# Kernel tuning notes

Hardware: AMD Instinct MI355X
Metric: run time of the kernel (lower is better)

The kernel has to match this reference:

```python
import jax, jax.numpy as jnp
import numpy as np

N_NODES = 50000
N_EDGES = 400000
IN_DIM = 512
OUT_DIM = 128
EPS = 1e-12  # F.normalize eps


def setup_inputs() -> dict:
    key = jax.random.key(0)
    ks = jax.random.split(key, 8)
    x = jax.random.normal(ks[0], (N_NODES, IN_DIM), dtype=jnp.float32)
    edge_index = jax.random.randint(ks[1], (2, N_EDGES), 0, N_NODES, dtype=jnp.int64)
    def glorot(k, fan_in, fan_out):
        s = jnp.sqrt(6.0 / (fan_in + fan_out)).astype(jnp.float32)
        return jax.random.uniform(k, (fan_in, fan_out), jnp.float32, -s, s)
    return {
        "x": x,
        "edge_index": edge_index,
        "W1": glorot(ks[2], IN_DIM, 512), "b1": jnp.zeros((512,), jnp.float32),
        "W2": glorot(ks[3], 512, 256),    "b2": jnp.zeros((256,), jnp.float32),
        "W3": glorot(ks[4], 256, OUT_DIM), "b3": jnp.zeros((OUT_DIM,), jnp.float32),
    }


def _gcn_layer(x, W, b, src, dst, dinv):
    # PyG GCNConv: h = x @ W; propagate with sym-norm D^-1/2 (A+I) D^-1/2; out += bias
    h = x @ W                                   # [N, F_out] dense GEMM (compute core)
    coef = dinv[src] * dinv[dst]                # [E]
    msg = h[src] * coef[:, None]                # gather + scale  [E, F_out]
    agg = jnp.zeros_like(h).at[dst].add(msg)    # scatter-add over destination nodes
    agg = agg + h * (dinv * dinv)[:, None]      # self-loop contribution
    return agg + b


def reference(x, edge_index, W1, b1, W2, b2, W3, b3):
    src, dst = edge_index[0], edge_index[1]
    n = x.shape[0]
    # degree with self-loops: deg[i] = 1 + in-degree(i)
    deg = jnp.ones((n,), x.dtype).at[dst].add(1.0)
    dinv = jax.lax.rsqrt(deg)
    # eval mode: F.dropout(training=False) is identity
    z = jax.nn.relu(_gcn_layer(x, W1, b1, src, dst, dinv))
    z = jax.nn.relu(_gcn_layer(z, W2, b2, src, dst, dinv))
    z = jax.nn.relu(_gcn_layer(z, W3, b3, src, dst, dinv))
    z = z / jnp.sum(z)
    z = jnp.tanh(z) ** 2
    norm = jnp.maximum(jnp.linalg.norm(z, axis=1, keepdims=True), EPS)
    return z / norm
```

## Files before the change

kernel.cpp:

```cpp
#include <hip/hip_runtime.h>
#include <math.h>

#define NN 50000
#define NE 400000
#define SLOTS 48
#define MT 391
#define BXPG 49

typedef unsigned short u16;
typedef __bf16 bf16x8 __attribute__((ext_vector_type(8)));
typedef float f32x4 __attribute__((ext_vector_type(4)));
typedef u16 bfu8 __attribute__((ext_vector_type(8)));
typedef u16 bfu4 __attribute__((ext_vector_type(4)));

__device__ __forceinline__ u16 f2bf(float f) {
    unsigned u = __builtin_bit_cast(unsigned, f);
    u += 0x7fff + ((u >> 16) & 1);
    return (u16)(u >> 16);
}
__device__ __forceinline__ float bf2f(u16 h) {
    unsigned u = ((unsigned)h) << 16;
    return __builtin_bit_cast(float, u);
}
__device__ __forceinline__ bfu8 cvt8(const float4& a, const float4& b) {
    bfu8 o;
    o[0] = f2bf(a.x); o[1] = f2bf(a.y); o[2] = f2bf(a.z); o[3] = f2bf(a.w);
    o[4] = f2bf(b.x); o[5] = f2bf(b.y); o[6] = f2bf(b.z); o[7] = f2bf(b.w);
    return o;
}

__device__ __forceinline__ void gload_lds16(const void* g, void* l) {
    typedef __attribute__((address_space(1))) const unsigned int GU;
    typedef __attribute__((address_space(3))) unsigned int LU;
    __builtin_amdgcn_global_load_lds((GU*)g, (LU*)l, 16, 0, 0);
}

__global__ void cvt_w(const float* __restrict__ W1, u16* __restrict__ Wt1,
                      const float* __restrict__ W2, u16* __restrict__ Wt2,
                      const float* __restrict__ W3, u16* __restrict__ Wt3) {
    int idx = blockIdx.x * blockDim.x + threadIdx.x;
    if (idx < 262144) {
        int n = idx >> 9, k = idx & 511;
        Wt1[idx] = f2bf(W1[(size_t)k * 512 + n]);
        return;
    }
    idx -= 262144;
    if (idx < 131072) {
        int n = idx >> 9, k = idx & 511;
        Wt2[idx] = f2bf(W2[(size_t)k * 256 + n]);
        return;
    }
    idx -= 131072;
    if (idx < 32768) {
        int n = idx >> 8, k = idx & 255;
        Wt3[idx] = f2bf(W3[(size_t)k * 128 + n]);
    }
}

__global__ void init_ell(int* __restrict__ ell, int* __restrict__ cnt, int N) {
    int i = blockIdx.x * blockDim.x + threadIdx.x;
    if (i < N * SLOTS) ell[i] = N;
    if (i < N) cnt[i] = 0;
}

__global__ void build_ell(const int* __restrict__ src, const int* __restrict__ dst,
                          int* __restrict__ cnt, int* __restrict__ ell, int E) {
    int e = blockIdx.x * blockDim.x + threadIdx.x;
    if (e < E) {
        const int d = dst[e];
        int pos = atomicAdd(&cnt[d], 1);
        if (pos < SLOTS) ell[d * SLOTS + pos] = src[e];
    }
}

__global__ void make_dinv(const int* __restrict__ cnt, float* __restrict__ dinv, int N) {
    int i = blockIdx.x * blockDim.x + threadIdx.x;
    if (i < N) dinv[i] = rsqrtf(1.0f + (float)cnt[i]);
    if (i == 0) dinv[N] = 0.f;
}

template <int NT, int CVT>
__global__ __launch_bounds__(256) void gemm_bf16(
    const void* __restrict__ Xv, const u16* __restrict__ Wt,
    u16* __restrict__ H, int N, int K, int NO)
{
    const int k8 = blockIdx.x & 7;
    const int idx = blockIdx.x >> 3;
    const int bx = k8 * BXPG + idx / NT;
    const int nt = idx - (idx / NT) * NT;
    const int m0 = bx * 128;
    if (m0 >= N) return;
    const int n0 = nt * 128;

    const u16* X = (const u16*)Xv;
    const float* Xf = (const float*)Xv;

    __shared__ unsigned char lds[33792];
    const int tid = threadIdx.x;
    const int w = tid >> 6;
    const int lane = tid & 63;

    f32x4 acc[4][4] = {};

    int gcol[2];
    int agrow[2], bgrow[2];
    #pragma unroll
    for (int i = 0; i < 2; ++i) {
        int idx2 = i * 256 + tid;
        int r = idx2 >> 2;
        int s = (idx2 & 3) ^ (r & 3);
        gcol[i] = s * 8;
        int ag = m0 + r; if (ag >= N) ag = N - 1;
        agrow[i] = ag;
        bgrow[i] = n0 + r;
    }

    float4 fa[2][2];
    #pragma unroll
    for (int i = 0; i < 2; ++i) {
        if constexpr (CVT) {
            const float* p = Xf + (size_t)agrow[i] * K + gcol[i];
            fa[i][0] = *reinterpret_cast<const float4*>(p);
            fa[i][1] = *reinterpret_cast<const float4*>(p + 4);
        } else {
            gload_lds16(X + (size_t)agrow[i] * K + gcol[i],
                        lds + i * 4096 + w * 1024);
        }
        gload_lds16(Wt + (size_t)bgrow[i] * K + gcol[i],
                    lds + 8192 + i * 4096 + w * 1024);
    }
    asm volatile("s_waitcnt vmcnt(0)" ::: "memory");
    if constexpr (CVT) {
        #pragma unroll
        for (int i = 0; i < 2; ++i)
            *reinterpret_cast<bfu8*>(lds + i * 4096 + (size_t)tid * 16) =
                cvt8(fa[i][0], fa[i][1]);
    }
    __syncthreads();

    int cur = 0;
    for (int k0 = 0; k0 < K; k0 += 32) {
        const bool more = (k0 + 32 < K);
        const int nb = (cur ^ 1) * 16384;
        if (more) {
            #pragma unroll
            for (int i = 0; i < 2; ++i) {
                if constexpr (CVT) {
                    const float* p = Xf + (size_t)agrow[i] * K + k0 + 32 + gcol[i];
                    fa[i][0] = *reinterpret_cast<const float4*>(p);
                    fa[i][1] = *reinterpret_cast<const float4*>(p + 4);
                } else {
                    gload_lds16(X + (size_t)agrow[i] * K + k0 + 32 + gcol[i],
                                lds + nb + i * 4096 + w * 1024);
                }
                gload_lds16(Wt + (size_t)bgrow[i] * K + k0 + 32 + gcol[i],
                            lds + nb + 8192 + i * 4096 + w * 1024);
            }
        }

        const int cb = cur * 16384;
        bf16x8 af[4], bfr[4];
        #pragma unroll
        for (int m = 0; m < 4; ++m) {
            int r = (w >> 1) * 64 + m * 16 + (lane & 15);
            int off = cb + r * 64 + (((lane >> 4) ^ (r & 3)) * 16);
            af[m] = *reinterpret_cast<const bf16x8*>(lds + off);
        }
        #pragma unroll
        for (int n = 0; n < 4; ++n) {
            int r = (w & 1) * 64 + n * 16 + (lane & 15);
            int off = cb + 8192 + r * 64 + (((lane >> 4) ^ (r & 3)) * 16);
            bfr[n] = *reinterpret_cast<const bf16x8*>(lds + off);
        }
        #pragma unroll
        for (int m = 0; m < 4; ++m)
            #pragma unroll
            for (int n = 0; n < 4; ++n)
                acc[m][n] = __builtin_amdgcn_mfma_f32_16x16x32_bf16(
                    af[m], bfr[n], acc[m][n], 0, 0, 0);

        asm volatile("s_waitcnt vmcnt(0)" ::: "memory");
        if (more) {
            if constexpr (CVT) {
                #pragma unroll
                for (int i = 0; i < 2; ++i)
                    *reinterpret_cast<bfu8*>(lds + nb + i * 4096 + (size_t)tid * 16) =
                        cvt8(fa[i][0], fa[i][1]);
            }
        }
        __syncthreads();
        cur ^= 1;
    }

    float* Cs = reinterpret_cast<float*>(lds);
    #pragma unroll
    for (int c = 0; c < 2; ++c) {
        __syncthreads();
        if ((w & 1) == c) {
            const int rbase = (w >> 1) * 64;
            #pragma unroll
            for (int m = 0; m < 4; ++m)
                #pragma unroll
                for (int n = 0; n < 4; ++n)
                    #pragma unroll
                    for (int r = 0; r < 4; ++r) {
                        int row = rbase + m * 16 + (lane >> 4) * 4 + r;
                        int col = n * 16 + (lane & 15);
                        Cs[row * 66 + col] = acc[m][n][r];
                    }
        }
        __syncthreads();
        const int row = tid >> 1;
        const int half = tid & 1;
        const int grow = m0 + row;
        if (grow < N) {
            const float* p = Cs + row * 66 + half * 32;
            bfu8 o0, o1, o2, o3;
            #pragma unroll
            for (int j = 0; j < 8; ++j) o0[j] = f2bf(p[j]);
            #pragma unroll
            for (int j = 0; j < 8; ++j) o1[j] = f2bf(p[8 + j]);
            #pragma unroll
            for (int j = 0; j < 8; ++j) o2[j] = f2bf(p[16 + j]);
            #pragma unroll
            for (int j = 0; j < 8; ++j) o3[j] = f2bf(p[24 + j]);
            bfu8* dst = reinterpret_cast<bfu8*>(H + (size_t)grow * NO + n0 + c * 64 + half * 32);
            dst[0] = o0; dst[1] = o1; dst[2] = o2; dst[3] = o3;
        }
    }
}

template <int F, int LPN, bool BFOUT, bool SUMOUT>
__global__ __launch_bounds__(128) void aggregate_bf(
    const u16* __restrict__ H, const int* __restrict__ cnt,
    const int* __restrict__ ell, const float* __restrict__ dinv,
    const float* __restrict__ bias, void* __restrict__ Aout,
    float* __restrict__ partials, int N)
{
    constexpr int EPL = F / LPN;
    const int gtid = blockIdx.x * blockDim.x + threadIdx.x;
    const int node = gtid / LPN;
    const int lane = gtid - node * LPN;
    const int co = lane * EPL;
    const bool valid = node < N;

    float a0[EPL], a1[EPL], a2[EPL], a3[EPL];
    #pragma unroll
    for (int q = 0; q < EPL; ++q) { a0[q] = 0.f; a1[q] = 0.f; a2[q] = 0.f; a3[q] = 0.f; }

    if (valid) {
        const int base = node * SLOTS;
        const int c = min(cnt[node], SLOTS);
        const int pd = (c + 3) & ~3;
        for (int j = 0; j < pd; j += 4) {
            const int4 s4 = *reinterpret_cast<const int4*>(ell + base + j);
            const float d0 = dinv[s4.x];
            const float d1 = dinv[s4.y];
            const float d2 = dinv[s4.z];
            const float d3 = dinv[s4.w];
            if constexpr (EPL == 8) {
                bfu8 v0 = *reinterpret_cast<const bfu8*>(H + (size_t)s4.x * F + co);
                bfu8 v1 = *reinterpret_cast<const bfu8*>(H + (size_t)s4.y * F + co);
                bfu8 v2 = *reinterpret_cast<const bfu8*>(H + (size_t)s4.z * F + co);
                bfu8 v3 = *reinterpret_cast<const bfu8*>(H + (size_t)s4.w * F + co);
                #pragma unroll
                for (int q = 0; q < 8; ++q) {
                    a0[q] = fmaf(bf2f(v0[q]), d0, a0[q]);
                    a1[q] = fmaf(bf2f(v1[q]), d1, a1[q]);
                    a2[q] = fmaf(bf2f(v2[q]), d2, a2[q]);
                    a3[q] = fmaf(bf2f(v3[q]), d3, a3[q]);
                }
            } else {
                bfu4 v0 = *reinterpret_cast<const bfu4*>(H + (size_t)s4.x * F + co);
                bfu4 v1 = *reinterpret_cast<const bfu4*>(H + (size_t)s4.y * F + co);
                bfu4 v2 = *reinterpret_cast<const bfu4*>(H + (size_t)s4.z * F + co);
                bfu4 v3 = *reinterpret_cast<const bfu4*>(H + (size_t)s4.w * F + co);
                #pragma unroll
                for (int q = 0; q < EPL; ++q) {
                    a0[q] = fmaf(bf2f(v0[q]), d0, a0[q]);
                    a1[q] = fmaf(bf2f(v1[q]), d1, a1[q]);
                    a2[q] = fmaf(bf2f(v2[q]), d2, a2[q]);
                    a3[q] = fmaf(bf2f(v3[q]), d3, a3[q]);
                }
            }
        }
    }

    float r[EPL];
    #pragma unroll
    for (int q = 0; q < EPL; ++q) r[q] = 0.f;
    if (valid) {
        const float dd = dinv[node], dd2 = dd * dd;
        if constexpr (EPL == 8) {
            bfu8 sv = *reinterpret_cast<const bfu8*>(H + (size_t)node * F + co);
            #pragma unroll
            for (int q = 0; q < 8; ++q)
                r[q] = fmaf((a0[q] + a1[q]) + (a2[q] + a3[q]), dd,
                            fmaf(bf2f(sv[q]), dd2, bias[co + q]));
        } else {
            bfu4 sv = *reinterpret_cast<const bfu4*>(H + (size_t)node * F + co);
            #pragma unroll
            for (int q = 0; q < EPL; ++q)
                r[q] = fmaf((a0[q] + a1[q]) + (a2[q] + a3[q]), dd,
                            fmaf(bf2f(sv[q]), dd2, bias[co + q]));
        }
    }

    if constexpr (BFOUT) {
        if (valid) {
            u16* out = reinterpret_cast<u16*>(Aout) + (size_t)node * F + co;
            if constexpr (EPL == 8) {
                bfu8 o;
                #pragma unroll
                for (int q = 0; q < 8; ++q) o[q] = f2bf(fmaxf(r[q], 0.f));
                *reinterpret_cast<bfu8*>(out) = o;
            } else {
                bfu4 o;
                #pragma unroll
                for (int q = 0; q < EPL; ++q) o[q] = f2bf(fmaxf(r[q], 0.f));
                *reinterpret_cast<bfu4*>(out) = o;
            }
        }
    } else if constexpr (SUMOUT) {
        float ls = 0.f;
        if (valid) {
            float* out = reinterpret_cast<float*>(Aout) + (size_t)node * F + co;
            #pragma unroll
            for (int q = 0; q < EPL; ++q) {
                const float z = fmaxf(r[q], 0.f);
                out[q] = z;
                ls += z;
            }
        }
        const int wl = threadIdx.x & 63, wi = threadIdx.x >> 6;
        #pragma unroll
        for (int off = 32; off; off >>= 1) ls += __shfl_down(ls, off);
        __shared__ float wsum[2];
        if (wl == 0) wsum[wi] = ls;
        __syncthreads();
        if (threadIdx.x == 0)
            partials[blockIdx.x] = wsum[0] + wsum[1];
    } else {
        if (valid) {
            float* out = reinterpret_cast<float*>(Aout) + (size_t)node * F + co;
            #pragma unroll
            for (int q = 0; q < EPL; ++q) out[q] = r[q];
        }
    }
}

__global__ __launch_bounds__(1024) void reduce_partials(const float* __restrict__ partials,
                                                        float* __restrict__ S, int n) {
    float local = 0.f;
    for (int i = threadIdx.x; i < n; i += 1024) local += partials[i];
    const int lane = threadIdx.x & 63, wid = threadIdx.x >> 6;
    #pragma unroll
    for (int off = 32; off; off >>= 1) local += __shfl_down(local, off);
    __shared__ float wsum[16];
    if (lane == 0) wsum[wid] = local;
    __syncthreads();
    if (threadIdx.x == 0) {
        float t = 0.f;
        #pragma unroll
        for (int i = 0; i < 16; ++i) t += wsum[i];
        *S = t;
    }
}

__global__ void final_norm(float* __restrict__ Z, const float* __restrict__ S, int N) {
    const int wid = threadIdx.x >> 6;
    const int lane = threadIdx.x & 63;
    const int row = blockIdx.x * 4 + wid;
    if (row >= N) return;
    const float inv = 1.0f / (*S);
    float v0 = Z[(size_t)row * 128 + lane] * inv;
    float v1 = Z[(size_t)row * 128 + lane + 64] * inv;
    const float t0 = tanhf(v0), t1 = tanhf(v1);
    const float y0 = t0 * t0, y1 = t1 * t1;
    float ss = y0 * y0 + y1 * y1;
    #pragma unroll
    for (int off = 32; off; off >>= 1) ss += __shfl_xor(ss, off);
    const float nrm = fmaxf(sqrtf(ss), 1e-12f);
    const float innrm = 1.0f / nrm;
    Z[(size_t)row * 128 + lane]      = y0 * innrm;
    Z[(size_t)row * 128 + lane + 64] = y1 * innrm;
}

extern "C" void kernel_launch(void* const* d_in, const int* in_sizes, int n_in,
                              void* d_out, int out_size, void* d_ws, size_t ws_size,
                              hipStream_t stream) {
    const float* x  = (const float*)d_in[0];
    const int*   ei = (const int*)d_in[1];
    const float* W1 = (const float*)d_in[2];
    const float* b1 = (const float*)d_in[3];
    const float* W2 = (const float*)d_in[4];
    const float* b2 = (const float*)d_in[5];
    const float* W3 = (const float*)d_in[6];
    const float* b3 = (const float*)d_in[7];
    float* out = (float*)d_out;

    const int N = NN, E = NE;
    const int* src = ei;
    const int* dst = ei + E;

    char* ws = (char*)d_ws;
    size_t off = 0;
    u16* bufA = (u16*)(ws + off); off += (size_t)(N + 1) * 512 * 2;
    u16* bufB = (u16*)(ws + off); off += (size_t)(N + 1) * 512 * 2;
    u16* Wt1 = (u16*)(ws + off); off += 512 * 512 * 2;
    u16* Wt2 = (u16*)(ws + off); off += 256 * 512 * 2;
    u16* Wt3 = (u16*)(ws + off); off += 128 * 256 * 2;
    float* dinv   = (float*)(ws + off); off += 204800;
    int*   cnt    = (int*)  (ws + off); off += 204800;
    float* Ssum   = (float*)(ws + off); off += 256;
    float* partials = (float*)(ws + off); off += 65536;
    int*   ell    = (int*)  (ws + off); off += (size_t)N * SLOTS * 4 + 256;

    cvt_w<<<(262144 + 131072 + 32768 + 255) / 256, 256, 0, stream>>>(
        W1, Wt1, W2, Wt2, W3, Wt3);

    init_ell<<<(N * SLOTS + 255) / 256, 256, 0, stream>>>(ell, cnt, N);
    build_ell<<<(E + 255) / 256, 256, 0, stream>>>(src, dst, cnt, ell, E);
    make_dinv<<<(N + 255) / 256, 256, 0, stream>>>(cnt, dinv, N);

    gemm_bf16<4, 1><<<8 * BXPG * 4, 256, 0, stream>>>(x, Wt1, bufB, N, 512, 512);
    aggregate_bf<512, 64, true, false><<<(N * 64 + 127) / 128, 128, 0, stream>>>(
        bufB, cnt, ell, dinv, b1, bufA, nullptr, N);
    gemm_bf16<2, 0><<<8 * BXPG * 2, 256, 0, stream>>>(bufA, Wt2, bufB, N, 512, 256);
    aggregate_bf<256, 32, true, false><<<(N * 32 + 127) / 128, 128, 0, stream>>>(
        bufB, cnt, ell, dinv, b2, bufA, nullptr, N);
    gemm_bf16<1, 0><<<8 * BXPG * 1, 256, 0, stream>>>(bufA, Wt3, bufB, N, 256, 128);
    const int aggBlocks3 = (N * 16 + 127) / 128;
    aggregate_bf<128, 16, false, true><<<aggBlocks3, 128, 0, stream>>>(
        bufB, cnt, ell, dinv, b3, out, partials, N);

    reduce_partials<<<1, 1024, 0, stream>>>(partials, Ssum, aggBlocks3);
    final_norm<<<(N + 3) / 4, 256, 0, stream>>>(out, Ssum, N);
}
```

Before: 275.4 us.

## Deepen fp32 input prefetch in first GEMM and make K a template constant

The first-layer GEMM, which converts fp32 input to bf16 on the fly, now loads fp32 activations two K-steps ahead into alternating register sets. It uses partial vmcnt waits, lgkmcnt plus s_barrier in place of full syncthreads, and a fully unrolled K loop. K becomes a compile-time template parameter for all GEMMs so loops and address math can be constant-folded. This aims to hide global-load latency in the largest GEMM, at the cost of more registers, which may lower occupancy, and delicate counter-based synchronisation.

```diff
diff --git a/kernel.cpp b/kernel.cpp
--- a/kernel.cpp
+++ b/kernel.cpp
@@ -79,11 +79,12 @@
     if (i == 0) dinv[N] = 0.f;
 }
 
-template <int NT, int CVT>
+template <int NT, int CVT, int KK>
 __global__ __launch_bounds__(256) void gemm_bf16(
     const void* __restrict__ Xv, const u16* __restrict__ Wt,
-    u16* __restrict__ H, int N, int K, int NO)
+    u16* __restrict__ H, int N, int NO)
 {
+    constexpr int NK = KK / 32;
     const int k8 = blockIdx.x & 7;
     const int idx = blockIdx.x >> 3;
     const int bx = k8 * BXPG + idx / NT;
@@ -115,81 +116,151 @@
         bgrow[i] = n0 + r;
     }
 
-    float4 fa[2][2];
-    #pragma unroll
-    for (int i = 0; i < 2; ++i) {
-        if constexpr (CVT) {
-            const float* p = Xf + (size_t)agrow[i] * K + gcol[i];
-            fa[i][0] = *reinterpret_cast<const float4*>(p);
-            fa[i][1] = *reinterpret_cast<const float4*>(p + 4);
-        } else {
-            gload_lds16(X + (size_t)agrow[i] * K + gcol[i],
-                        lds + i * 4096 + w * 1024);
-        }
-        gload_lds16(Wt + (size_t)bgrow[i] * K + gcol[i],
-                    lds + 8192 + i * 4096 + w * 1024);
-    }
-    asm volatile("s_waitcnt vmcnt(0)" ::: "memory");
     if constexpr (CVT) {
+        float4 fa0[2][2], fa1[2][2];
+        #pragma unroll
+        for (int i = 0; i < 2; ++i) {
+            gload_lds16(Wt + (size_t)bgrow[i] * KK + gcol[i],
+                        lds + 8192 + i * 4096 + w * 1024);
+            const float* p = Xf + (size_t)agrow[i] * KK + gcol[i];
+            fa0[i][0] = *reinterpret_cast<const float4*>(p);
+            fa0[i][1] = *reinterpret_cast<const float4*>(p + 4);
+        }
+        asm volatile("s_waitcnt vmcnt(0)" ::: "memory");
         #pragma unroll
         for (int i = 0; i < 2; ++i)
             *reinterpret_cast<bfu8*>(lds + i * 4096 + (size_t)tid * 16) =
-                cvt8(fa[i][0], fa[i][1]);
-    }
-    __syncthreads();
-
-    int cur = 0;
-    for (int k0 = 0; k0 < K; k0 += 32) {
-        const bool more = (k0 + 32 < K);
-        const int nb = (cur ^ 1) * 16384;
-        if (more) {
+                cvt8(fa0[i][0], fa0[i][1]);
+        asm volatile("s_waitcnt lgkmcnt(0)" ::: "memory");
+        __builtin_amdgcn_s_barrier();
+        if constexpr (NK > 1) {
             #pragma unroll
             for (int i = 0; i < 2; ++i) {
-                if constexpr (CVT) {
-                    const float* p = Xf + (size_t)agrow[i] * K + k0 + 32 + gcol[i];
-                    fa[i][0] = *reinterpret_cast<const float4*>(p);
-                    fa[i][1] = *reinterpret_cast<const float4*>(p + 4);
+                gload_lds16(Wt + (size_t)bgrow[i] * KK + 32 + gcol[i],
+                            lds + 16384 + 8192 + i * 4096 + w * 1024);
+                const float* p = Xf + (size_t)agrow[i] * KK + 32 + gcol[i];
+                fa0[i][0] = *reinterpret_cast<const float4*>(p);
+                fa0[i][1] = *reinterpret_cast<const float4*>(p + 4);
+            }
+        }
+
+        #pragma unroll
+        for (int k = 0; k < NK; ++k) {
+            const int cb = (k & 1) * 16384;
+            bf16x8 af[4], bfr[4];
+            #pragma unroll
+            for (int m = 0; m < 4; ++m) {
+                int r = (w >> 1) * 64 + m * 16 + (lane & 15);
+                int off = cb + r * 64 + (((lane >> 4) ^ (r & 3)) * 16);
+                af[m] = *reinterpret_cast<const bf16x8*>(lds + off);
+            }
+            #pragma unroll
+            for (int n = 0; n < 4; ++n) {
+                int r = (w & 1) * 64 + n * 16 + (lane & 15);
+                int off = cb + 8192 + r * 64 + (((lane >> 4) ^ (r & 3)) * 16);
+                bfr[n] = *reinterpret_cast<const bf16x8*>(lds + off);
+            }
+            if (k + 2 < NK) {
+                if ((k & 1) == 0) {
+                    #pragma unroll
+                    for (int i = 0; i < 2; ++i) {
+                        const float* p = Xf + (size_t)agrow[i] * KK + (k + 2) * 32 + gcol[i];
+                        fa1[i][0] = *reinterpret_cast<const float4*>(p);
+                        fa1[i][1] = *reinterpret_cast<const float4*>(p + 4);
+                    }
                 } else {
-                    gload_lds16(X + (size_t)agrow[i] * K + k0 + 32 + gcol[i],
+                    #pragma unroll
+                    for (int i = 0; i < 2; ++i) {
+                        const float* p = Xf + (size_t)agrow[i] * KK + (k + 2) * 32 + gcol[i];
+                        fa0[i][0] = *reinterpret_cast<const float4*>(p);
+                        fa0[i][1] = *reinterpret_cast<const float4*>(p + 4);
+                    }
+                }
+            }
+            #pragma unroll
+            for (int m = 0; m < 4; ++m)
+                #pragma unroll
+                for (int n = 0; n < 4; ++n)
+                    acc[m][n] = __builtin_amdgcn_mfma_f32_16x16x32_bf16(
+                        af[m], bfr[n], acc[m][n], 0, 0, 0);
+
+            if (k < NK - 1) {
+                if (k + 2 < NK) {
+                    asm volatile("s_waitcnt vmcnt(4)" ::: "memory");
+                } else {
+                    asm volatile("s_waitcnt vmcnt(0)" ::: "memory");
+                }
+                const int nb = ((k & 1) ^ 1) * 16384;
+                if ((k & 1) == 0) {
+                    #pragma unroll
+                    for (int i = 0; i < 2; ++i)
+                        *reinterpret_cast<bfu8*>(lds + nb + i * 4096 + (size_t)tid * 16) =
+                            cvt8(fa0[i][0], fa0[i][1]);
+                } else {
+                    #pragma unroll
+                    for (int i = 0; i < 2; ++i)
+                        *reinterpret_cast<bfu8*>(lds + nb + i * 4096 + (size_t)tid * 16) =
+                            cvt8(fa1[i][0], fa1[i][1]);
+                }
+                asm volatile("s_waitcnt lgkmcnt(0)" ::: "memory");
+                __builtin_amdgcn_s_barrier();
+                if (k + 2 < NK) {
+                    #pragma unroll
+                    for (int i = 0; i < 2; ++i)
+                        gload_lds16(Wt + (size_t)bgrow[i] * KK + (k + 2) * 32 + gcol[i],
+                                    lds + cb + 8192 + i * 4096 + w * 1024);
+                }
+            }
+        }
+    } else {
+        #pragma unroll
+        for (int i = 0; i < 2; ++i) {
+            gload_lds16(X + (size_t)agrow[i] * KK + gcol[i],
+                        lds + i * 4096 + w * 1024);
+            gload_lds16(Wt + (size_t)bgrow[i] * KK + gcol[i],
+                        lds + 8192 + i * 4096 + w * 1024);
+        }
+        asm volatile("s_waitcnt vmcnt(0)" ::: "memory");
+        __syncthreads();
+
+        int cur = 0;
+        for (int k0 = 0; k0 < KK; k0 += 32) {
+            const bool more = (k0 + 32 < KK);
+            const int nb = (cur ^ 1) * 16384;
+            if (more) {
+                #pragma unroll
+                for (int i = 0; i < 2; ++i) {
+                    gload_lds16(X + (size_t)agrow[i] * KK + k0 + 32 + gcol[i],
                                 lds + nb + i * 4096 + w * 1024);
-                }
-                gload_lds16(Wt + (size_t)bgrow[i] * K + k0 + 32 + gcol[i],
-                            lds + nb + 8192 + i * 4096 + w * 1024);
-            }
-        }
-
-        const int cb = cur * 16384;
-        bf16x8 af[4], bfr[4];
-        #pragma unroll
-        for (int m = 0; m < 4; ++m) {
-            int r = (w >> 1) * 64 + m * 16 + (lane & 15);
-            int off = cb + r * 64 + (((lane >> 4) ^ (r & 3)) * 16);
-            af[m] = *reinterpret_cast<const bf16x8*>(lds + off);
-        }
-        #pragma unroll
-        for (int n = 0; n < 4; ++n) {
-            int r = (w & 1) * 64 + n * 16 + (lane & 15);
-            int off = cb + 8192 + r * 64 + (((lane >> 4) ^ (r & 3)) * 16);
-            bfr[n] = *reinterpret_cast<const bf16x8*>(lds + off);
-        }
-        #pragma unroll
-        for (int m = 0; m < 4; ++m)
-            #pragma unroll
-            for (int n = 0; n < 4; ++n)
-                acc[m][n] = __builtin_amdgcn_mfma_f32_16x16x32_bf16(
-                    af[m], bfr[n], acc[m][n], 0, 0, 0);
-
-        asm volatile("s_waitcnt vmcnt(0)" ::: "memory");
-        if (more) {
-            if constexpr (CVT) {
-                #pragma unroll
-                for (int i = 0; i < 2; ++i)
-                    *reinterpret_cast<bfu8*>(lds + nb + i * 4096 + (size_t)tid * 16) =
-                        cvt8(fa[i][0], fa[i][1]);
-            }
-        }
-        __syncthreads();
-        cur ^= 1;
+                    gload_lds16(Wt + (size_t)bgrow[i] * KK + k0 + 32 + gcol[i],
+                                lds + nb + 8192 + i * 4096 + w * 1024);
+                }
+            }
+            const int cb = cur * 16384;
+            bf16x8 af[4], bfr[4];
+            #pragma unroll
+            for (int m = 0; m < 4; ++m) {
+                int r = (w >> 1) * 64 + m * 16 + (lane & 15);
+                int off = cb + r * 64 + (((lane >> 4) ^ (r & 3)) * 16);
+                af[m] = *reinterpret_cast<const bf16x8*>(lds + off);
+            }
+            #pragma unroll
+            for (int n = 0; n < 4; ++n) {
+                int r = (w & 1) * 64 + n * 16 + (lane & 15);
+                int off = cb + 8192 + r * 64 + (((lane >> 4) ^ (r & 3)) * 16);
+                bfr[n] = *reinterpret_cast<const bf16x8*>(lds + off);
+            }
+            #pragma unroll
+            for (int m = 0; m < 4; ++m)
+                #pragma unroll
+                for (int n = 0; n < 4; ++n)
+                    acc[m][n] = __builtin_amdgcn_mfma_f32_16x16x32_bf16(
+                        af[m], bfr[n], acc[m][n], 0, 0, 0);
+
+            asm volatile("s_waitcnt vmcnt(0)" ::: "memory");
+            __syncthreads();
+            cur ^= 1;
+        }
     }
 
     float* Cs = reinterpret_cast<float*>(lds);
@@ -423,13 +494,13 @@
     build_ell<<<(E + 255) / 256, 256, 0, stream>>>(src, dst, cnt, ell, E);
     make_dinv<<<(N + 255) / 256, 256, 0, stream>>>(cnt, dinv, N);
 
-    gemm_bf16<4, 1><<<8 * BXPG * 4, 256, 0, stream>>>(x, Wt1, bufB, N, 512, 512);
+    gemm_bf16<4, 1, 512><<<8 * BXPG * 4, 256, 0, stream>>>(x, Wt1, bufB, N, 512);
     aggregate_bf<512, 64, true, false><<<(N * 64 + 127) / 128, 128, 0, stream>>>(
         bufB, cnt, ell, dinv, b1, bufA, nullptr, N);
-    gemm_bf16<2, 0><<<8 * BXPG * 2, 256, 0, stream>>>(bufA, Wt2, bufB, N, 512, 256);
+    gemm_bf16<2, 0, 512><<<8 * BXPG * 2, 256, 0, stream>>>(bufA, Wt2, bufB, N, 256);
     aggregate_bf<256, 32, true, false><<<(N * 32 + 127) / 128, 128, 0, stream>>>(
         bufB, cnt, ell, dinv, b2, bufA, nullptr, N);
-    gemm_bf16<1, 0><<<8 * BXPG * 1, 256, 0, stream>>>(bufA, Wt3, bufB, N, 256, 128);
+    gemm_bf16<1, 0, 256><<<8 * BXPG * 1, 256, 0, stream>>>(bufA, Wt3, bufB, N, 128);
     const int aggBlocks3 = (N * 16 + 127) / 128;
     aggregate_bf<128, 16, false, true><<<aggBlocks3, 128, 0, stream>>>(
         bufB, cnt, ell, dinv, b3, out, partials, N);
```

Measured after the change: 281.5 us. 2.2% more time.

## Load fp32 X tiles directly to LDS and convert to bf16 at fragment read

Applied to the files above, without the earlier changes.

The first-layer GEMM used to load fp32 activations into registers, convert them to bf16 and store them to LDS. It now streams the fp32 tile straight into a larger LDS buffer with async global_load_lds, using an XOR swizzle over 8 chunks. The bf16 conversion happens on each fragment read with v_cvt_pk_bf16_f32, which removes the register round-trip and the extra LDS write from the critical path. K also becomes a compile-time template parameter. The cost is more LDS per block (48 KB vs 33 KB), which may reduce occupancy, and conversion work that is repeated by the wave pairs sharing the same A rows.

```diff
diff --git a/kernel.cpp b/kernel.cpp
--- a/kernel.cpp
+++ b/kernel.cpp
@@ -10,6 +10,7 @@
 typedef unsigned short u16;
 typedef __bf16 bf16x8 __attribute__((ext_vector_type(8)));
 typedef float f32x4 __attribute__((ext_vector_type(4)));
+typedef unsigned int u32x4 __attribute__((ext_vector_type(4)));
 typedef u16 bfu8 __attribute__((ext_vector_type(8)));
 typedef u16 bfu4 __attribute__((ext_vector_type(4)));
 
@@ -21,12 +22,6 @@
 __device__ __forceinline__ float bf2f(u16 h) {
     unsigned u = ((unsigned)h) << 16;
     return __builtin_bit_cast(float, u);
-}
-__device__ __forceinline__ bfu8 cvt8(const float4& a, const float4& b) {
-    bfu8 o;
-    o[0] = f2bf(a.x); o[1] = f2bf(a.y); o[2] = f2bf(a.z); o[3] = f2bf(a.w);
-    o[4] = f2bf(b.x); o[5] = f2bf(b.y); o[6] = f2bf(b.z); o[7] = f2bf(b.w);
-    return o;
 }
 
 __device__ __forceinline__ void gload_lds16(const void* g, void* l) {
@@ -79,10 +74,10 @@
     if (i == 0) dinv[N] = 0.f;
 }
 
-template <int NT, int CVT>
+template <int NT, int CVT, int KK>
 __global__ __launch_bounds__(256) void gemm_bf16(
     const void* __restrict__ Xv, const u16* __restrict__ Wt,
-    u16* __restrict__ H, int N, int K, int NO)
+    u16* __restrict__ H, int N, int NO)
 {
     const int k8 = blockIdx.x & 7;
     const int idx = blockIdx.x >> 3;
@@ -95,7 +90,7 @@
     const u16* X = (const u16*)Xv;
     const float* Xf = (const float*)Xv;
 
-    __shared__ unsigned char lds[33792];
+    __shared__ unsigned char lds[CVT ? 49152 : 33792];
     const int tid = threadIdx.x;
     const int w = tid >> 6;
     const int lane = tid & 63;
@@ -115,81 +110,127 @@
         bgrow[i] = n0 + r;
     }
 
-    float4 fa[2][2];
-    #pragma unroll
-    for (int i = 0; i < 2; ++i) {
-        if constexpr (CVT) {
-            const float* p = Xf + (size_t)agrow[i] * K + gcol[i];
-            fa[i][0] = *reinterpret_cast<const float4*>(p);
-            fa[i][1] = *reinterpret_cast<const float4*>(p + 4);
-        } else {
-            gload_lds16(X + (size_t)agrow[i] * K + gcol[i],
+    if constexpr (CVT) {
+        const int gcolf = (((tid & 7) ^ ((tid >> 3) & 7)) << 2);
+        int agrow4[4];
+        #pragma unroll
+        for (int i = 0; i < 4; ++i) {
+            int rr = m0 + ((i * 256 + tid) >> 3);
+            agrow4[i] = (rr < N) ? rr : N - 1;
+        }
+
+        #pragma unroll
+        for (int i = 0; i < 4; ++i)
+            gload_lds16(Xf + (size_t)agrow4[i] * KK + gcolf,
                         lds + i * 4096 + w * 1024);
-        }
-        gload_lds16(Wt + (size_t)bgrow[i] * K + gcol[i],
-                    lds + 8192 + i * 4096 + w * 1024);
-    }
-    asm volatile("s_waitcnt vmcnt(0)" ::: "memory");
-    if constexpr (CVT) {
         #pragma unroll
         for (int i = 0; i < 2; ++i)
-            *reinterpret_cast<bfu8*>(lds + i * 4096 + (size_t)tid * 16) =
-                cvt8(fa[i][0], fa[i][1]);
-    }
-    __syncthreads();
-
-    int cur = 0;
-    for (int k0 = 0; k0 < K; k0 += 32) {
-        const bool more = (k0 + 32 < K);
-        const int nb = (cur ^ 1) * 16384;
-        if (more) {
-            #pragma unroll
-            for (int i = 0; i < 2; ++i) {
-                if constexpr (CVT) {
-                    const float* p = Xf + (size_t)agrow[i] * K + k0 + 32 + gcol[i];
-                    fa[i][0] = *reinterpret_cast<const float4*>(p);
-                    fa[i][1] = *reinterpret_cast<const float4*>(p + 4);
-                } else {
-                    gload_lds16(X + (size_t)agrow[i] * K + k0 + 32 + gcol[i],
+            gload_lds16(Wt + (size_t)bgrow[i] * KK + gcol[i],
+                        lds + 32768 + i * 4096 + w * 1024);
+        asm volatile("s_waitcnt vmcnt(0)" ::: "memory");
+        __syncthreads();
+
+        int cur = 0;
+        for (int k0 = 0; k0 < KK; k0 += 32) {
+            const bool more = (k0 + 32 < KK);
+            if (more) {
+                const int na = (cur ^ 1) * 16384;
+                const int nb = 32768 + (cur ^ 1) * 8192;
+                #pragma unroll
+                for (int i = 0; i < 4; ++i)
+                    gload_lds16(Xf + (size_t)agrow4[i] * KK + k0 + 32 + gcolf,
+                                lds + na + i * 4096 + w * 1024);
+                #pragma unroll
+                for (int i = 0; i < 2; ++i)
+                    gload_lds16(Wt + (size_t)bgrow[i] * KK + k0 + 32 + gcol[i],
                                 lds + nb + i * 4096 + w * 1024);
+            }
+
+            const int ca = cur * 16384;
+            const int cbb = 32768 + cur * 8192;
+            bf16x8 af[4], bfr[4];
+            #pragma unroll
+            for (int m = 0; m < 4; ++m) {
+                const int r = (w >> 1) * 64 + m * 16 + (lane & 15);
+                const int g = lane >> 4;
+                const int j0 = (2 * g) ^ (r & 7);
+                const int j1 = (2 * g + 1) ^ (r & 7);
+                const f32x4 lo = *reinterpret_cast<const f32x4*>(lds + ca + r * 128 + j0 * 16);
+                const f32x4 hi = *reinterpret_cast<const f32x4*>(lds + ca + r * 128 + j1 * 16);
+                unsigned q0, q1, q2, q3;
+                asm("v_cvt_pk_bf16_f32 %0, %1, %2" : "=v"(q0) : "v"(lo[0]), "v"(lo[1]));
+                asm("v_cvt_pk_bf16_f32 %0, %1, %2" : "=v"(q1) : "v"(lo[2]), "v"(lo[3]));
+                asm("v_cvt_pk_bf16_f32 %0, %1, %2" : "=v"(q2) : "v"(hi[0]), "v"(hi[1]));
+                asm("v_cvt_pk_bf16_f32 %0, %1, %2" : "=v"(q3) : "v"(hi[2]), "v"(hi[3]));
+                u32x4 t; t[0] = q0; t[1] = q1; t[2] = q2; t[3] = q3;
+                af[m] = __builtin_bit_cast(bf16x8, t);
+            }
+            #pragma unroll
+            for (int n = 0; n < 4; ++n) {
+                const int r = (w & 1) * 64 + n * 16 + (lane & 15);
+                const int off = cbb + r * 64 + (((lane >> 4) ^ (r & 3)) * 16);
+                bfr[n] = *reinterpret_cast<const bf16x8*>(lds + off);
+            }
+            #pragma unroll
+            for (int m = 0; m < 4; ++m)
+                #pragma unroll
+                for (int n = 0; n < 4; ++n)
+                    acc[m][n] = __builtin_amdgcn_mfma_f32_16x16x32_bf16(
+                        af[m], bfr[n], acc[m][n], 0, 0, 0);
+
+            asm volatile("s_waitcnt vmcnt(0)" ::: "memory");
+            __syncthreads();
+            cur ^= 1;
+        }
+    } else {
+        #pragma unroll
+        for (int i = 0; i < 2; ++i) {
+            gload_lds16(X + (size_t)agrow[i] * KK + gcol[i],
+                        lds + i * 4096 + w * 1024);
+            gload_lds16(Wt + (size_t)bgrow[i] * KK + gcol[i],
+                        lds + 8192 + i * 4096 + w * 1024);
+        }
+        asm volatile("s_waitcnt vmcnt(0)" ::: "memory");
+        __syncthreads();
+
+        int cur = 0;
+        for (int k0 = 0; k0 < KK; k0 += 32) {
+            const bool more = (k0 + 32 < KK);
+            const int nb = (cur ^ 1) * 16384;
+            if (more) {
+                #pragma unroll
+                for (int i = 0; i < 2; ++i) {
+                    gload_lds16(X + (size_t)agrow[i] * KK + k0 + 32 + gcol[i],
+                                lds + nb + i * 4096 + w * 1024);
+                    gload_lds16(Wt + (size_t)bgrow[i] * KK + k0 + 32 + gcol[i],
+                                lds + nb + 8192 + i * 4096 + w * 1024);
                 }
-                gload_lds16(Wt + (size_t)bgrow[i] * K + k0 + 32 + gcol[i],
-                            lds + nb + 8192 + i * 4096 + w * 1024);
-            }
-        }
-
-        const int cb = cur * 16384;
-        bf16x8 af[4], bfr[4];
-        #pragma unroll
-        for (int m = 0; m < 4; ++m) {
-            int r = (w >> 1) * 64 + m * 16 + (lane & 15);
-            int off = cb + r * 64 + (((lane >> 4) ^ (r & 3)) * 16);
-            af[m] = *reinterpret_cast<const bf16x8*>(lds + off);
-        }
-        #pragma unroll
-        for (int n = 0; n < 4; ++n) {
-            int r = (w & 1) * 64 + n * 16 + (lane & 15);
-            int off = cb + 8192 + r * 64 + (((lane >> 4) ^ (r & 3)) * 16);
-            bfr[n] = *reinterpret_cast<const bf16x8*>(lds + off);
-        }
-        #pragma unroll
-        for (int m = 0; m < 4; ++m)
-            #pragma unroll
-            for (int n = 0; n < 4; ++n)
-                acc[m][n] = __builtin_amdgcn_mfma_f32_16x16x32_bf16(
-                    af[m], bfr[n], acc[m][n], 0, 0, 0);
-
-        asm volatile("s_waitcnt vmcnt(0)" ::: "memory");
-        if (more) {
-            if constexpr (CVT) {
-                #pragma unroll
-                for (int i = 0; i < 2; ++i)
-                    *reinterpret_cast<bfu8*>(lds + nb + i * 4096 + (size_t)tid * 16) =
-                        cvt8(fa[i][0], fa[i][1]);
-            }
-        }
-        __syncthreads();
-        cur ^= 1;
+            }
+            const int cb = cur * 16384;
+            bf16x8 af[4], bfr[4];
+            #pragma unroll
+            for (int m = 0; m < 4; ++m) {
+                int r = (w >> 1) * 64 + m * 16 + (lane & 15);
+                int off = cb + r * 64 + (((lane >> 4) ^ (r & 3)) * 16);
+                af[m] = *reinterpret_cast<const bf16x8*>(lds + off);
+            }
+            #pragma unroll
+            for (int n = 0; n < 4; ++n) {
+                int r = (w & 1) * 64 + n * 16 + (lane & 15);
+                int off = cb + 8192 + r * 64 + (((lane >> 4) ^ (r & 3)) * 16);
+                bfr[n] = *reinterpret_cast<const bf16x8*>(lds + off);
+            }
+            #pragma unroll
+            for (int m = 0; m < 4; ++m)
+                #pragma unroll
+                for (int n = 0; n < 4; ++n)
+                    acc[m][n] = __builtin_amdgcn_mfma_f32_16x16x32_bf16(
+                        af[m], bfr[n], acc[m][n], 0, 0, 0);
+
+            asm volatile("s_waitcnt vmcnt(0)" ::: "memory");
+            __syncthreads();
+            cur ^= 1;
+        }
     }
 
     float* Cs = reinterpret_cast<float*>(lds);
@@ -423,13 +464,13 @@
     build_ell<<<(E + 255) / 256, 256, 0, stream>>>(src, dst, cnt, ell, E);
     make_dinv<<<(N + 255) / 256, 256, 0, stream>>>(cnt, dinv, N);
 
-    gemm_bf16<4, 1><<<8 * BXPG * 4, 256, 0, stream>>>(x, Wt1, bufB, N, 512, 512);
+    gemm_bf16<4, 1, 512><<<8 * BXPG * 4, 256, 0, stream>>>(x, Wt1, bufB, N, 512);
     aggregate_bf<512, 64, true, false><<<(N * 64 + 127) / 128, 128, 0, stream>>>(
         bufB, cnt, ell, dinv, b1, bufA, nullptr, N);
-    gemm_bf16<2, 0><<<8 * BXPG * 2, 256, 0, stream>>>(bufA, Wt2, bufB, N, 512, 256);
+    gemm_bf16<2, 0, 512><<<8 * BXPG * 2, 256, 0, stream>>>(bufA, Wt2, bufB, N, 256);
     aggregate_bf<256, 32, true, false><<<(N * 32 + 127) / 128, 128, 0, stream>>>(
         bufB, cnt, ell, dinv, b2, bufA, nullptr, N);
-    gemm_bf16<1, 0><<<8 * BXPG * 1, 256, 0, stream>>>(bufA, Wt3, bufB, N, 256, 128);
+    gemm_bf16<1, 0, 256><<<8 * BXPG * 1, 256, 0, stream>>>(bufA, Wt3, bufB, N, 128);
     const int aggBlocks3 = (N * 16 + 127) / 128;
     aggregate_bf<128, 16, false, true><<<aggBlocks3, 128, 0, stream>>>(
         bufB, cnt, ell, dinv, b3, out, partials, N);
```

Measured after the change: 274.4 us. Within noise of the previous version (-0.4%).
